# Kernel optimization log

Hardware: AMD Instinct MI355X
Metric: run time of the kernel (lower is better)

Reference implementation:

```python
import jax, jax.numpy as jnp
import numpy as np

B, S, H, NH = 2, 2048, 768, 12
HD = H // NH  # 64


def setup_inputs() -> dict:
    key = jax.random.key(0)
    ks = jax.random.split(key, 4)
    scale = 1.0 / np.sqrt(H)
    return {
        "hidden_states": jax.random.normal(ks[0], (B, S, H), dtype=jnp.float32),
        "Wq": jax.random.normal(ks[1], (H, H), dtype=jnp.float32) * scale,
        "bq": jnp.zeros((H,), dtype=jnp.float32),
        "Wk": jax.random.normal(ks[2], (H, H), dtype=jnp.float32) * scale,
        "bk": jnp.zeros((H,), dtype=jnp.float32),
        "Wv": jax.random.normal(ks[3], (H, H), dtype=jnp.float32) * scale,
        "bv": jnp.zeros((H,), dtype=jnp.float32),
    }


def _split_heads(x):
    # [B,S,H] -> [B,NH,S,HD]  (transpose_for_scores)
    b, s, _ = x.shape
    return x.reshape(b, s, NH, HD).transpose(0, 2, 1, 3)


def reference(hidden_states, Wq, bq, Wk, bk, Wv, bv):
    q = _split_heads(hidden_states @ Wq + bq)  # [B,NH,S,HD]
    k = _split_heads(hidden_states @ Wk + bk)
    v = _split_heads(hidden_states @ Wv + bv)
    # delegated attn_fn(q,k,v): scaled-dot-product softmax attention
    scores = jnp.einsum("bhqd,bhkd->bhqk", q, k) / jnp.sqrt(jnp.asarray(HD, q.dtype))
    probs = jax.nn.softmax(scores, axis=-1)
    ctx = jnp.einsum("bhqk,bhkd->bhqd", probs, v)  # [B,NH,S,HD]
    # merge heads back: permute(0,2,1,3) then view to [B,S,H]
    out = ctx.transpose(0, 2, 1, 3).reshape(B, S, NH * HD)
    return out
```

## Files before the change

kernel.cpp:

```cpp
#include <hip/hip_runtime.h>
#include <stdint.h>

typedef __bf16 bf16_t;
typedef __bf16 bf16x8 __attribute__((ext_vector_type(8)));
typedef float f32x4 __attribute__((ext_vector_type(4)));
typedef float f32x16 __attribute__((ext_vector_type(16)));

#define DEV __device__ __forceinline__

DEV void gload_lds16(const void* g, void* lds) {
  __builtin_amdgcn_global_load_lds(
      (const __attribute__((address_space(1))) uint32_t*)g,
      (__attribute__((address_space(3))) uint32_t*)lds, 16, 0, 0);
}

DEV float fexp2(float x) {
#if __has_builtin(__builtin_amdgcn_exp2f)
  return __builtin_amdgcn_exp2f(x);
#else
  return exp2f(x);
#endif
}

DEV uint32_t pk_bf16(float a, float b) {
  uint32_t lo = (uint32_t)__builtin_bit_cast(uint16_t, (bf16_t)a);
  uint32_t hi = (uint32_t)__builtin_bit_cast(uint16_t, (bf16_t)b);
  return lo | (hi << 16);
}

__global__ __launch_bounds__(256) void prep(const float* __restrict__ hs,
                                            const float* __restrict__ Wq,
                                            const float* __restrict__ Wk,
                                            const float* __restrict__ Wv,
                                            bf16_t* __restrict__ hsb,
                                            bf16_t* __restrict__ WT) {
  const int bx = blockIdx.x;
  if (bx < 3072) {
    int i = bx * 256 + threadIdx.x;
    float4 v = ((const float4*)hs)[i];
    ((uint2*)hsb)[i] = make_uint2(pk_bf16(v.x, v.y), pk_bf16(v.z, v.w));
    return;
  }
  __shared__ float T[32][36];
  const int bx2 = bx - 3072;
  const int wn = bx2 % 72;
  const int wk = bx2 / 72;
  const int p = wn / 24;
  const float* W = (p == 0) ? Wq : ((p == 1) ? Wk : Wv);
  const int n0 = wn * 32, nn0 = n0 - p * 768, k0 = wk * 32;
  const int t = threadIdx.x;
  {
    int r = t >> 3, c4 = (t & 7) * 4;
    float4 v = *(const float4*)&W[(size_t)(k0 + r) * 768 + nn0 + c4];
    T[r][c4 + 0] = v.x; T[r][c4 + 1] = v.y; T[r][c4 + 2] = v.z; T[r][c4 + 3] = v.w;
  }
  __syncthreads();
  {
    int nr = t >> 3, kc = (t & 7) * 4;
    uint32_t lo = pk_bf16(T[kc + 0][nr], T[kc + 1][nr]);
    uint32_t hi = pk_bf16(T[kc + 2][nr], T[kc + 3][nr]);
    *(uint2*)&WT[(size_t)(n0 + nr) * 768 + k0 + kc] = make_uint2(lo, hi);
  }
}

__global__ __launch_bounds__(256) void gemm_qkv(
    const bf16_t* __restrict__ A, const bf16_t* __restrict__ Wt,
    const float* __restrict__ bq, const float* __restrict__ bk,
    const float* __restrict__ bv, bf16_t* __restrict__ Qf,
    bf16_t* __restrict__ Kf, bf16_t* __restrict__ Vf) {
  __shared__ __align__(16) char smem[34816];
  bf16_t* As = (bf16_t*)smem;
  bf16_t* Bs = As + 128 * 64;
  bf16_t* Cs = (bf16_t*)smem;
  const int bx = blockIdx.x;
  const int by = blockIdx.y;
  const int m0 = by * 128, n0 = bx * 128;
  const int tid = threadIdx.x, w = tid >> 6, lane = tid & 63;
  const int mw = (w & 1) * 64, nw = (w >> 1) * 64;
  const int quad = lane >> 4, col = lane & 15;

  f32x4 acc[4][4];
  for (int i = 0; i < 4; i++)
    for (int j = 0; j < 4; j++) acc[i][j] = (f32x4){0.f, 0.f, 0.f, 0.f};

  const int srow = w * 32 + (lane >> 3);
  const int scol = (lane & 7) * 8;
  const bf16_t* ag = A + (size_t)(m0 + srow) * 768 + scol;
  const bf16_t* bg = Wt + (size_t)(n0 + srow) * 768 + scol;

  for (int kk = 0; kk < 12; ++kk) {
    const int k0 = kk * 64;
    __syncthreads();
#pragma unroll
    for (int i = 0; i < 4; i++) {
      gload_lds16(ag + (size_t)i * 8 * 768 + k0, As + (w * 32 + i * 8) * 64);
      gload_lds16(bg + (size_t)i * 8 * 768 + k0, Bs + (w * 32 + i * 8) * 64);
    }
    __syncthreads();
#pragma unroll
    for (int ks = 0; ks < 2; ++ks) {
      bf16x8 af[4], bf[4];
#pragma unroll
      for (int mt = 0; mt < 4; ++mt)
        af[mt] = *(const bf16x8*)&As[(mw + mt * 16 + col) * 64 + ks * 32 + quad * 8];
#pragma unroll
      for (int nt = 0; nt < 4; ++nt)
        bf[nt] = *(const bf16x8*)&Bs[(nw + nt * 16 + col) * 64 + ks * 32 + quad * 8];
#pragma unroll
      for (int mt = 0; mt < 4; ++mt)
#pragma unroll
        for (int nt = 0; nt < 4; ++nt)
          acc[mt][nt] = __builtin_amdgcn_mfma_f32_16x16x32_bf16(
              af[mt], bf[nt], acc[mt][nt], 0, 0, 0);
    }
  }

  const int p = bx / 6;
  const float* bp = (p == 0) ? bq : ((p == 1) ? bk : bv);
  const float kscale = (p == 1) ? 0.18033688011112042f : 1.0f;
  const int bb0 = m0 >> 11, s0 = m0 & 2047;
  const int lq2 = tid & 31, hf = (tid >> 5) & 1, lblk = tid >> 6;
  __syncthreads();
  if (p < 2) {
#pragma unroll
    for (int nt = 0; nt < 4; nt++) {
      int n = nw + nt * 16 + col;
      float bias = bp[n0 + n - p * 768];
#pragma unroll
      for (int mt = 0; mt < 4; mt++)
#pragma unroll
        for (int r = 0; r < 4; r++) {
          int m = mw + mt * 16 + quad * 4 + r;
          Cs[m * 136 + n] = (bf16_t)((acc[mt][nt][r] + bias) * kscale);
        }
    }
    __syncthreads();
    bf16_t* dst = (p == 0) ? Qf : Kf;
#pragma unroll
    for (int pass = 0; pass < 8; pass++) {
      int blkid = pass * 4 + lblk;
      int head_l = blkid >> 4, g = (blkid >> 2) & 3, ks = blkid & 3;
      bf16x8 v = *(const bf16x8*)&Cs[(g * 32 + lq2) * 136 + head_l * 64 + ks * 16 + hf * 8];
      int headg = (n0 - p * 768) / 64 + head_l;
      int qtl = (s0 >> 6) + (g >> 1), qt2 = g & 1;
      size_t blk = ((size_t)((bb0 * 12 + headg) * 32 + qtl) * 2 + qt2) * 4 + ks;
      *(bf16x8*)&dst[blk * 512 + (size_t)(tid & 63) * 8] = v;
    }
  } else {
#pragma unroll
    for (int nt = 0; nt < 4; nt++) {
      int n = nw + nt * 16 + col;
      float bias = bp[n0 + n - 1536];
#pragma unroll
      for (int mt = 0; mt < 4; mt++)
#pragma unroll
        for (int r = 0; r < 4; r++) {
          int m = mw + mt * 16 + quad * 4 + r;
          Cs[n * 136 + m] = (bf16_t)(acc[mt][nt][r] + bias);
        }
    }
    __syncthreads();
#pragma unroll
    for (int pass = 0; pass < 8; pass++) {
      int blkid = pass * 4 + lblk;
      int head_l = blkid >> 4, kbl = (blkid >> 3) & 1, dt = (blkid >> 2) & 1, c = blkid & 3;
      bf16x8 v = *(const bf16x8*)&Cs[(head_l * 64 + dt * 32 + lq2) * 136 + kbl * 64 + c * 16 + hf * 8];
      int headg = (n0 - 1536) / 64 + head_l;
      int kb = (s0 >> 6) + kbl;
      size_t blk = ((size_t)((bb0 * 12 + headg) * 32 + kb) * 2 + dt) * 4 + c;
      *(bf16x8*)&Vf[blk * 512 + (size_t)(tid & 63) * 8] = v;
    }
  }
}

__global__ __launch_bounds__(64, 1) void attn(const bf16_t* __restrict__ Qf,
                                              const bf16_t* __restrict__ Kf,
                                              const bf16_t* __restrict__ Vf,
                                              float* __restrict__ out) {
  __shared__ float Of[64 * 68];
  const int bh = blockIdx.x;
  const int qtl = blockIdx.y;
  const int b = bh / 12, head = bh % 12;
  const int lane = threadIdx.x, lq = lane & 31, half = lane >> 5;

  bf16x8 qf[2][4];
  {
    const bf16_t* qb = Qf + ((size_t)(bh * 32 + qtl) * 8) * 512 + lane * 8;
#pragma unroll
    for (int qt2 = 0; qt2 < 2; qt2++)
#pragma unroll
      for (int ks = 0; ks < 4; ks++)
        qf[qt2][ks] = *(const bf16x8*)(qb + (qt2 * 4 + ks) * 512);
  }

  f32x16 oacc[2][2];
  for (int i = 0; i < 16; i++) {
    oacc[0][0][i] = 0.f; oacc[0][1][i] = 0.f;
    oacc[1][0][i] = 0.f; oacc[1][1][i] = 0.f;
  }
  float l_own[2] = {0.f, 0.f};

  const bf16_t* kp0 = Kf + (size_t)bh * 32 * 8 * 512 + lane * 8;
  const bf16_t* vp0 = Vf + (size_t)bh * 32 * 8 * 512 + lane * 8;

  bf16x8 kf[2][8], vf[2][8];

  auto loadKV = [&](int kb, int bb) {
    const bf16_t* kp = kp0 + (size_t)kb * 8 * 512;
    const bf16_t* vp = vp0 + (size_t)kb * 8 * 512;
#pragma unroll
    for (int i = 0; i < 8; i++) {
      kf[bb][i] = *(const bf16x8*)(kp + i * 512);
      vf[bb][i] = *(const bf16x8*)(vp + i * 512);
    }
  };

  auto compute = [&](int bb) {
    f32x16 sacc[2][2];
    for (int i = 0; i < 16; i++) {
      sacc[0][0][i] = 0.f; sacc[0][1][i] = 0.f;
      sacc[1][0][i] = 0.f; sacc[1][1][i] = 0.f;
    }
#pragma unroll
    for (int ks = 0; ks < 4; ++ks)
#pragma unroll
      for (int t = 0; t < 2; t++) {
        sacc[t][0] = __builtin_amdgcn_mfma_f32_32x32x16_bf16(kf[bb][t * 4 + ks], qf[0][ks], sacc[t][0], 0, 0, 0);
        sacc[t][1] = __builtin_amdgcn_mfma_f32_32x32x16_bf16(kf[bb][t * 4 + ks], qf[1][ks], sacc[t][1], 0, 0, 0);
      }

#pragma unroll
    for (int qt2 = 0; qt2 < 2; qt2++)
#pragma unroll
      for (int t = 0; t < 2; t++)
#pragma unroll
        for (int r = 0; r < 16; r++) {
          float pv = fexp2(sacc[t][qt2][r]);
          sacc[t][qt2][r] = pv;
          l_own[qt2] += pv;
        }

    bf16x8 pfrag[2][4];
#pragma unroll
    for (int qt2 = 0; qt2 < 2; qt2++) {
      uint32_t pk[2][4][2];
#pragma unroll
      for (int t = 0; t < 2; t++)
#pragma unroll
        for (int g = 0; g < 4; g++) {
          pk[t][g][0] = pk_bf16(sacc[t][qt2][4 * g + 0], sacc[t][qt2][4 * g + 1]);
          pk[t][g][1] = pk_bf16(sacc[t][qt2][4 * g + 2], sacc[t][qt2][4 * g + 3]);
        }
#pragma unroll
      for (int t = 0; t < 2; t++)
#pragma unroll
        for (int e = 0; e < 2; e++) {
          uint32_t s0 = half ? pk[t][2 * e][0] : pk[t][2 * e + 1][0];
          uint32_t s1 = half ? pk[t][2 * e][1] : pk[t][2 * e + 1][1];
          uint32_t r0 = __shfl_xor(s0, 32);
          uint32_t r1 = __shfl_xor(s1, 32);
          uint32_t o0 = half ? pk[t][2 * e + 1][0] : pk[t][2 * e][0];
          uint32_t o1 = half ? pk[t][2 * e + 1][1] : pk[t][2 * e][1];
          union { uint32_t u[4]; bf16x8 v; } F;
          F.u[0] = half ? r0 : o0;
          F.u[1] = half ? r1 : o1;
          F.u[2] = half ? o0 : r0;
          F.u[3] = half ? o1 : r1;
          pfrag[qt2][2 * t + e] = F.v;
        }
    }

#pragma unroll
    for (int c = 0; c < 4; c++)
#pragma unroll
      for (int dt = 0; dt < 2; dt++) {
        oacc[dt][0] = __builtin_amdgcn_mfma_f32_32x32x16_bf16(vf[bb][dt * 4 + c], pfrag[0][c], oacc[dt][0], 0, 0, 0);
        oacc[dt][1] = __builtin_amdgcn_mfma_f32_32x32x16_bf16(vf[bb][dt * 4 + c], pfrag[1][c], oacc[dt][1], 0, 0, 0);
      }
  };

  loadKV(0, 0);
  for (int kk = 0; kk < 16; ++kk) {
    loadKV(2 * kk + 1, 1);
    compute(0);
    if (kk < 15) loadKV(2 * kk + 2, 0);
    compute(1);
  }

  float inv0, inv1;
  {
    float l0 = l_own[0] + __shfl_xor(l_own[0], 32);
    float l1 = l_own[1] + __shfl_xor(l_own[1], 32);
    inv0 = 1.0f / l0; inv1 = 1.0f / l1;
  }
#pragma unroll
  for (int dt = 0; dt < 2; dt++)
#pragma unroll
    for (int qt2 = 0; qt2 < 2; qt2++) {
      float inv = qt2 ? inv1 : inv0;
#pragma unroll
      for (int r = 0; r < 16; r++) {
        int d = dt * 32 + (r & 3) + 8 * (r >> 2) + 4 * half;
        int q = qt2 * 32 + lq;
        Of[q * 68 + (((d >> 2) ^ (q & 15)) * 4) + (d & 3)] = oacc[dt][qt2][r] * inv;
      }
    }
  float* ob = out + ((size_t)b * 2048 + qtl * 64) * 768 + head * 64;
#pragma unroll
  for (int i = 0; i < 16; i++) {
    int idx = i * 64 + lane;
    int q = idx >> 4, c = idx & 15;
    f32x4 v = *(f32x4*)&Of[q * 68 + ((c ^ (q & 15)) * 4)];
    *(f32x4*)&ob[(size_t)q * 768 + c * 4] = v;
  }
}

extern "C" void kernel_launch(void* const* d_in, const int* in_sizes, int n_in,
                              void* d_out, int out_size, void* d_ws, size_t ws_size,
                              hipStream_t stream) {
  const float* hs = (const float*)d_in[0];
  const float* Wq = (const float*)d_in[1];
  const float* bq = (const float*)d_in[2];
  const float* Wk = (const float*)d_in[3];
  const float* bk = (const float*)d_in[4];
  const float* Wv = (const float*)d_in[5];
  const float* bv = (const float*)d_in[6];
  float* out = (float*)d_out;

  char* w = (char*)d_ws;
  bf16_t* hsb = (bf16_t*)w; w += (size_t)4096 * 768 * 2;
  bf16_t* wtb = (bf16_t*)w; w += (size_t)2304 * 768 * 2;
  bf16_t* Qf  = (bf16_t*)w; w += (size_t)24 * 2048 * 64 * 2;
  bf16_t* Kf  = (bf16_t*)w; w += (size_t)24 * 2048 * 64 * 2;
  bf16_t* Vf  = (bf16_t*)w;

  hipLaunchKernelGGL(prep, dim3(4800), dim3(256), 0, stream, hs, Wq, Wk, Wv, hsb, wtb);
  hipLaunchKernelGGL(gemm_qkv, dim3(18, 32), dim3(256), 0, stream, hsb, wtb, bq,
                     bk, bv, Qf, Kf, Vf);
  hipLaunchKernelGGL(attn, dim3(24, 32), dim3(64), 0, stream, Qf, Kf, Vf, out);
}
```

Baseline: 173.0 us.

## Split attention key range across four waves per block with LDS reduction

```diff
diff --git a/kernel.cpp b/kernel.cpp
--- a/kernel.cpp
+++ b/kernel.cpp
@@ -173,15 +173,20 @@
   }
 }
 
-__global__ __launch_bounds__(64, 1) void attn(const bf16_t* __restrict__ Qf,
-                                              const bf16_t* __restrict__ Kf,
-                                              const bf16_t* __restrict__ Vf,
-                                              float* __restrict__ out) {
-  __shared__ float Of[64 * 68];
+__global__ __launch_bounds__(256, 2) void attn(const bf16_t* __restrict__ Qf,
+                                               const bf16_t* __restrict__ Kf,
+                                               const bf16_t* __restrict__ Vf,
+                                               float* __restrict__ out) {
+  __shared__ float Of[64 * 65];
+  __shared__ float Ll[64];
   const int bh = blockIdx.x;
   const int qtl = blockIdx.y;
   const int b = bh / 12, head = bh % 12;
-  const int lane = threadIdx.x, lq = lane & 31, half = lane >> 5;
+  const int tid = threadIdx.x, wv = tid >> 6, lane = tid & 63;
+  const int lq = lane & 31, half = lane >> 5;
+
+  for (int i = tid; i < 64 * 65; i += 256) Of[i] = 0.f;
+  if (tid < 64) Ll[tid] = 0.f;
 
   bf16x8 qf[2][4];
   {
@@ -200,14 +205,14 @@
   }
   float l_own[2] = {0.f, 0.f};
 
-  const bf16_t* kp0 = Kf + (size_t)bh * 32 * 8 * 512 + lane * 8;
-  const bf16_t* vp0 = Vf + (size_t)bh * 32 * 8 * 512 + lane * 8;
+  const bf16_t* kp0 = Kf + ((size_t)(bh * 32 + wv * 8)) * 4096 + lane * 8;
+  const bf16_t* vp0 = Vf + ((size_t)(bh * 32 + wv * 8)) * 4096 + lane * 8;
 
   bf16x8 kf[2][8], vf[2][8];
 
   auto loadKV = [&](int kb, int bb) {
-    const bf16_t* kp = kp0 + (size_t)kb * 8 * 512;
-    const bf16_t* vp = vp0 + (size_t)kb * 8 * 512;
+    const bf16_t* kp = kp0 + (size_t)kb * 4096;
+    const bf16_t* vp = vp0 + (size_t)kb * 4096;
 #pragma unroll
     for (int i = 0; i < 8; i++) {
       kf[bb][i] = *(const bf16x8*)(kp + i * 512);
@@ -279,38 +284,46 @@
       }
   };
 
+  __syncthreads();
+
   loadKV(0, 0);
-  for (int kk = 0; kk < 16; ++kk) {
+#pragma unroll 1
+  for (int kk = 0; kk < 4; ++kk) {
     loadKV(2 * kk + 1, 1);
     compute(0);
-    if (kk < 15) loadKV(2 * kk + 2, 0);
+    if (kk < 3) loadKV(2 * kk + 2, 0);
     compute(1);
   }
 
-  float inv0, inv1;
   {
     float l0 = l_own[0] + __shfl_xor(l_own[0], 32);
     float l1 = l_own[1] + __shfl_xor(l_own[1], 32);
-    inv0 = 1.0f / l0; inv1 = 1.0f / l1;
+    if (half == 0) {
+      atomicAdd(&Ll[lq], l0);
+      atomicAdd(&Ll[32 + lq], l1);
+    }
   }
 #pragma unroll
   for (int dt = 0; dt < 2; dt++)
 #pragma unroll
-    for (int qt2 = 0; qt2 < 2; qt2++) {
-      float inv = qt2 ? inv1 : inv0;
+    for (int qt2 = 0; qt2 < 2; qt2++)
 #pragma unroll
       for (int r = 0; r < 16; r++) {
         int d = dt * 32 + (r & 3) + 8 * (r >> 2) + 4 * half;
         int q = qt2 * 32 + lq;
-        Of[q * 68 + (((d >> 2) ^ (q & 15)) * 4) + (d & 3)] = oacc[dt][qt2][r] * inv;
+        atomicAdd(&Of[q * 65 + d], oacc[dt][qt2][r]);
       }
-    }
+  __syncthreads();
+
   float* ob = out + ((size_t)b * 2048 + qtl * 64) * 768 + head * 64;
 #pragma unroll
-  for (int i = 0; i < 16; i++) {
-    int idx = i * 64 + lane;
+  for (int i = 0; i < 4; i++) {
+    int idx = i * 256 + tid;
     int q = idx >> 4, c = idx & 15;
-    f32x4 v = *(f32x4*)&Of[q * 68 + ((c ^ (q & 15)) * 4)];
+    float inv = 1.0f / Ll[q];
+    f32x4 v;
+#pragma unroll
+    for (int j = 0; j < 4; j++) v[j] = Of[q * 65 + c * 4 + j] * inv;
     *(f32x4*)&ob[(size_t)q * 768 + c * 4] = v;
   }
 }
@@ -337,5 +350,5 @@
   hipLaunchKernelGGL(prep, dim3(4800), dim3(256), 0, stream, hs, Wq, Wk, Wv, hsb, wtb);
   hipLaunchKernelGGL(gemm_qkv, dim3(18, 32), dim3(256), 0, stream, hsb, wtb, bq,
                      bk, bv, Qf, Kf, Vf);
-  hipLaunchKernelGGL(attn, dim3(24, 32), dim3(64), 0, stream, Qf, Kf, Vf, out);
-}
+  hipLaunchKernelGGL(attn, dim3(24, 32), dim3(256), 0, stream, Qf, Kf, Vf, out);
+}
```

Result: slower. 239.1 us (+38.2%).
